# Kernel optimization log

Hardware: AMD Instinct MI355X
Metric: run time of the kernel (lower is better)

The kernel has to match this reference:

```python
import jax, jax.numpy as jnp
import numpy as np

N = 20000      # nodes
DEG = 16       # uniform in-degree (edges sorted by destination)
F_IN = 96      # raw node feature dim
T_EMB = 32     # node-type embedding dim -> conv1 input = 128
H = 128        # hidden_channels == out_channels
N_TYPES = 8


def _lstm_agg(x_seq, w_ih, w_hh, b_ih, b_hh):
    """LSTMAggregation: run LSTM over each node's neighbor sequence, return last hidden. x_seq: [N, T, F] -> [N, F]."""
    n = x_seq.shape[0]
    hdim = w_hh.shape[1]
    h0 = jnp.zeros((n, hdim), x_seq.dtype)
    bias = b_ih + b_hh

    def step(carry, x_t):
        h, c = carry
        gates = x_t @ w_ih.T + h @ w_hh.T + bias  # [N, 4H], torch gate order i,f,g,o
        i, f, g, o = jnp.split(gates, 4, axis=-1)
        i = jax.nn.sigmoid(i)
        f = jax.nn.sigmoid(f)
        g = jnp.tanh(g)
        o = jax.nn.sigmoid(o)
        c = f * c + i * g
        h = o * jnp.tanh(c)
        return (h, c), None

    (h, _), _ = jax.lax.scan(step, (h0, h0), jnp.swapaxes(x_seq, 0, 1))
    return h


def _sage_lstm(x, src, params):
    """SAGEConv with aggr='lstm': out = lin_l(LSTM_agg(x_j)) + lin_r(x)."""
    w_ih, w_hh, b_ih, b_hh, w_l, b_l, w_r = params
    # dst = repeat(arange(N), DEG) (sorted), so grouping neighbors per node is a reshape
    x_j = x[src].reshape(x.shape[0], DEG, x.shape[1])  # gather: [N, DEG, F]
    agg = _lstm_agg(x_j, w_ih, w_hh, b_ih, b_hh)
    return agg @ w_l.T + b_l + x @ w_r.T


def setup_inputs() -> dict:
    key = jax.random.key(0)
    ks = jax.random.split(key, 40)

    def rn(i, shape, s=0.05):
        return (jax.random.normal(ks[i], shape, jnp.float32) * s)

    inp = {
        "x": rn(0, (N, F_IN), 1.0),
        "node_type_ids": jax.random.randint(ks[1], (N,), 0, N_TYPES),
        "edge_src": jax.random.randint(ks[2], (N * DEG,), 0, N),
        "edge_dst": jnp.repeat(jnp.arange(N), DEG),
        "type_emb": rn(3, (N_TYPES, T_EMB)),
    }
    k = 4
    for l in (1, 2, 3):
        inp[f"w_ih{l}"] = rn(k, (4 * H, H)); k += 1
        inp[f"w_hh{l}"] = rn(k, (4 * H, H)); k += 1
        inp[f"b_ih{l}"] = rn(k, (4 * H,)); k += 1
        inp[f"b_hh{l}"] = rn(k, (4 * H,)); k += 1
        inp[f"w_l{l}"] = rn(k, (H, H)); k += 1
        inp[f"b_l{l}"] = rn(k, (H,)); k += 1
        inp[f"w_r{l}"] = rn(k, (H, H)); k += 1
    return inp


def reference(x, node_type_ids, edge_src, edge_dst, type_emb,
              w_ih1, w_hh1, b_ih1, b_hh1, w_l1, b_l1, w_r1,
              w_ih2, w_hh2, b_ih2, b_hh2, w_l2, b_l2, w_r2,
              w_ih3, w_hh3, b_ih3, b_hh3, w_l3, b_l3, w_r3):
    del edge_dst  # sortedness/uniform degree encoded in the reshape
    h = jnp.concatenate([x, type_emb[node_type_ids]], axis=1)  # [N, 128]
    h = jax.nn.relu(_sage_lstm(h, edge_src, (w_ih1, w_hh1, b_ih1, b_hh1, w_l1, b_l1, w_r1)))  # dropout = identity (eval)
    h = jax.nn.relu(_sage_lstm(h, edge_src, (w_ih2, w_hh2, b_ih2, b_hh2, w_l2, b_l2, w_r2)))
    h = _sage_lstm(h, edge_src, (w_ih3, w_hh3, b_ih3, b_hh3, w_l3, b_l3, w_r3))
    return h
```

## Files before the change

kernel.cpp:

```cpp
#include <hip/hip_runtime.h>

#define NN 20000
#define DEG 16
#define HDIM 128
#define GDIM 512

typedef __attribute__((ext_vector_type(8))) short bf16x8;
typedef __attribute__((ext_vector_type(4))) float f32x4;
typedef __attribute__((ext_vector_type(2))) unsigned u32x2;
typedef __attribute__((ext_vector_type(4))) unsigned u32x4;
typedef unsigned long long ull;

#define L2E  1.4426950408889634f
#define L2E2 2.8853900817779268f

__device__ __forceinline__ f32x4 mfma16(bf16x8 a, bf16x8 b, f32x4 c) {
    return __builtin_amdgcn_mfma_f32_16x16x32_bf16(a, b, c, 0, 0, 0);
}

__device__ __forceinline__ unsigned short f2bf(float f) {
    unsigned u = __builtin_bit_cast(unsigned, f);
    u += 0x7FFFu + ((u >> 16) & 1u);
    return (unsigned short)(u >> 16);
}

__device__ __forceinline__ unsigned cvtpk(float lo, float hi) {
    unsigned r;
    asm("v_cvt_pk_bf16_f32 %0, %1, %2" : "=v"(r) : "v"(lo), "v"(hi));
    return r;
}

__device__ __forceinline__ float bfhi(unsigned u) { return __builtin_bit_cast(float, u & 0xFFFF0000u); }
__device__ __forceinline__ float bflo(unsigned u) { return __builtin_bit_cast(float, u << 16); }

__device__ __forceinline__ void barrier_lgkm() {
    asm volatile("s_waitcnt lgkmcnt(0)\ns_barrier" ::: "memory");
}

__device__ __forceinline__ float sig_pre(float x) {
    return __builtin_amdgcn_rcpf(1.f + __builtin_amdgcn_exp2f(-x));
}
__device__ __forceinline__ float tanh_pre2(float x2) {
    return 1.f - 2.f * __builtin_amdgcn_rcpf(__builtin_amdgcn_exp2f(x2) + 1.f);
}

struct CvtArgs {
    const float *wih[3], *whh[3], *wl[3], *wr[3], *bih[3], *bhh[3];
    unsigned short *dih[3], *dhh[3], *dl[3], *dr[3];
    float *dbias[3];
};

__global__ __launch_bounds__(256) void cvt_kernel(CvtArgs a) {
    int l = blockIdx.x / 642, b = blockIdx.x % 642, t = threadIdx.x;
    if (b < 256) {
        int i = b * 256 + t;
        float s = ((i >> 14) == 2) ? L2E2 : L2E;
        a.dih[l][i] = f2bf(a.wih[l][i] * s);
    } else if (b < 512) {
        int i = (b - 256) * 256 + t;
        float s = ((i >> 14) == 2) ? L2E2 : L2E;
        a.dhh[l][i] = f2bf(a.whh[l][i] * s);
    } else if (b < 576) {
        int i = (b - 512) * 256 + t;
        a.dl[l][i] = f2bf(a.wl[l][i]);
    } else if (b < 640) {
        int i = (b - 576) * 256 + t;
        a.dr[l][i] = f2bf(a.wr[l][i]);
    } else {
        int i = (b - 640) * 256 + t;
        float s = ((i >> 7) == 2) ? L2E2 : L2E;
        a.dbias[l][i] = (a.bih[l][i] + a.bhh[l][i]) * s;
    }
}

__device__ __forceinline__ void phaseA2(const unsigned short (*htile)[136],
        const unsigned short* __restrict__ wih, const float* __restrict__ biasc,
        unsigned short* __restrict__ xihb, int mbase, int cl, int qh, int k8, int wv) {
    bf16x8 a0[4], a1[4];
#pragma unroll
    for (int kt = 0; kt < 4; ++kt) {
        a0[kt] = *(const bf16x8*)(&htile[cl][kt * 32 + k8]);
        a1[kt] = *(const bf16x8*)(&htile[16 + cl][kt * 32 + k8]);
    }
#pragma unroll
    for (int nt = 0; nt < 2; ++nt) {
        const int col = wv * 32 + nt * 16 + cl;
        f32x4 acc0[4], acc1[4];
#pragma unroll
        for (int g = 0; g < 4; ++g) {
            acc0[g] = (f32x4){0.f, 0.f, 0.f, 0.f};
            acc1[g] = (f32x4){0.f, 0.f, 0.f, 0.f};
        }
#pragma unroll
        for (int g = 0; g < 4; ++g)
#pragma unroll
            for (int kt = 0; kt < 4; ++kt) {
                bf16x8 b = *(const bf16x8*)(wih + (g * 128 + col) * HDIM + kt * 32 + k8);
                acc0[g] = mfma16(a0[kt], b, acc0[g]);
                acc1[g] = mfma16(a1[kt], b, acc1[g]);
            }
        float bias[4];
#pragma unroll
        for (int g = 0; g < 4; ++g) bias[g] = biasc[g * 128 + col];
#pragma unroll
        for (int r = 0; r < 4; ++r) {
            unsigned p0 = cvtpk(acc0[0][r] + bias[0], acc0[1][r] + bias[1]);
            unsigned p1 = cvtpk(acc0[2][r] + bias[2], acc0[3][r] + bias[3]);
            *(ull*)(xihb + (size_t)(mbase + qh * 4 + r) * GDIM + col * 4) =
                (ull)p0 | ((ull)p1 << 32);
            unsigned q0 = cvtpk(acc1[0][r] + bias[0], acc1[1][r] + bias[1]);
            unsigned q1 = cvtpk(acc1[2][r] + bias[2], acc1[3][r] + bias[3]);
            *(ull*)(xihb + (size_t)(mbase + 16 + qh * 4 + r) * GDIM + col * 4) =
                (ull)q0 | ((ull)q1 << 32);
        }
    }
}

__global__ __launch_bounds__(256) void gemmA0_kernel(
        const float* __restrict__ x, const int* __restrict__ types,
        const float* __restrict__ emb, const unsigned short* __restrict__ wih,
        const float* __restrict__ biasc, unsigned short* __restrict__ h0,
        unsigned short* __restrict__ xihb) {
    __shared__ unsigned short htile[32][136];
    const int tid = threadIdx.x;
    const int lane = tid & 63, wv = tid >> 6;
    const int cl = lane & 15, qh = lane >> 4, k8 = qh * 8;
    const int mbase = blockIdx.x * 32;

    const int row = tid >> 3, c0 = (tid & 7) * 16;
    f32x4 u[4];
    if (c0 < 96) {
#pragma unroll
        for (int j = 0; j < 4; ++j)
            u[j] = *(const f32x4*)(x + (size_t)(mbase + row) * 96 + c0 + 4 * j);
    } else {
        int ty = types[mbase + row];
#pragma unroll
        for (int j = 0; j < 4; ++j)
            u[j] = *(const f32x4*)(emb + ty * 32 + (c0 - 96) + 4 * j);
    }
    u32x4 pk, pk2;
    pk[0]  = cvtpk(u[0][0], u[0][1]); pk[1]  = cvtpk(u[0][2], u[0][3]);
    pk[2]  = cvtpk(u[1][0], u[1][1]); pk[3]  = cvtpk(u[1][2], u[1][3]);
    pk2[0] = cvtpk(u[2][0], u[2][1]); pk2[1] = cvtpk(u[2][2], u[2][3]);
    pk2[2] = cvtpk(u[3][0], u[3][1]); pk2[3] = cvtpk(u[3][2], u[3][3]);
    *(u32x4*)(&htile[row][c0]) = pk;
    *(u32x4*)(&htile[row][c0 + 8]) = pk2;
    *(u32x4*)(h0 + (size_t)(mbase + row) * HDIM + c0) = pk;
    *(u32x4*)(h0 + (size_t)(mbase + row) * HDIM + c0 + 8) = pk2;
    __syncthreads();

    phaseA2(htile, wih, biasc, xihb, mbase, cl, qh, k8, wv);
}

__global__ __launch_bounds__(512, 2) void lstm_kernel(
        const unsigned short* __restrict__ xihb, const unsigned short* __restrict__ whh,
        const int* __restrict__ esrc, unsigned short* __restrict__ agg) {
    __shared__ unsigned short hbuf[2][16][136];
    __shared__ unsigned srcs_t[256];

    const int tid = threadIdx.x;
    const int lane = tid & 63, wv = tid >> 6;
    const int cl = lane & 15, qh = lane >> 4, k8 = qh * 8;
    const int colb = wv * 16 + cl;
    const int base = blockIdx.x * 16;

    if (tid < 256)
        srcs_t[(tid & 15) * 16 + (tid >> 4)] = ((unsigned)esrc[base * DEG + tid]) << 10;

    const unsigned short* wp = whh + colb * HDIM + k8;
#define LDW(kt, g) (*(const bf16x8*)(wp + (g) * 128 * HDIM + (kt) * 32))
    bf16x8 w00 = LDW(0,0), w01 = LDW(0,1), w02 = LDW(0,2), w03 = LDW(0,3);
    bf16x8 w10 = LDW(1,0), w11 = LDW(1,1), w12 = LDW(1,2), w13 = LDW(1,3);
    bf16x8 w20 = LDW(2,0), w21 = LDW(2,1), w22 = LDW(2,2), w23 = LDW(2,3);
    bf16x8 w30 = LDW(3,0), w31 = LDW(3,1), w32 = LDW(3,2), w33 = LDW(3,3);
#undef LDW
    __syncthreads();

    const char* xp = (const char*)xihb + (size_t)colb * 8u;
    float c0 = 0.f, c1 = 0.f, c2 = 0.f, c3 = 0.f;
    unsigned pk0 = 0, pk1 = 0;
    ull xa0, xa1, xa2, xa3, xb0, xb1, xb2, xb3;

#define GATH(T, X0, X1, X2, X3) { \
    u32x4 sv = *(const u32x4*)&srcs_t[(T) * 16 + qh * 4]; \
    X0 = *(const ull*)(xp + sv[0]); \
    X1 = *(const ull*)(xp + sv[1]); \
    X2 = *(const ull*)(xp + sv[2]); \
    X3 = *(const ull*)(xp + sv[3]); }

    GATH(0, xa0, xa1, xa2, xa3)
    GATH(1, xb0, xb1, xb2, xb3)

#define STEP(T, X0, X1, X2, X3) { \
    f32x4 a0, a1, a2, a3; \
    { unsigned lo = (unsigned)X0, hi = (unsigned)(X0 >> 32); \
      a0[0] = bflo(lo); a1[0] = bfhi(lo); a2[0] = bflo(hi); a3[0] = bfhi(hi); } \
    { unsigned lo = (unsigned)X1, hi = (unsigned)(X1 >> 32); \
      a0[1] = bflo(lo); a1[1] = bfhi(lo); a2[1] = bflo(hi); a3[1] = bfhi(hi); } \
    { unsigned lo = (unsigned)X2, hi = (unsigned)(X2 >> 32); \
      a0[2] = bflo(lo); a1[2] = bfhi(lo); a2[2] = bflo(hi); a3[2] = bfhi(hi); } \
    { unsigned lo = (unsigned)X3, hi = (unsigned)(X3 >> 32); \
      a0[3] = bflo(lo); a1[3] = bfhi(lo); a2[3] = bflo(hi); a3[3] = bfhi(hi); } \
    if ((T) < 14) { GATH((T) + 2, X0, X1, X2, X3) } \
    if ((T) > 0) { \
        const unsigned short* hrow = &hbuf[((T) + 1) & 1][cl][k8]; \
        bf16x8 h0 = *(const bf16x8*)(hrow); \
        bf16x8 h1 = *(const bf16x8*)(hrow + 32); \
        bf16x8 h2 = *(const bf16x8*)(hrow + 64); \
        bf16x8 h3 = *(const bf16x8*)(hrow + 96); \
        a0 = mfma16(h0, w00, a0); a0 = mfma16(h1, w10, a0); \
        a0 = mfma16(h2, w20, a0); a0 = mfma16(h3, w30, a0); \
        a1 = mfma16(h0, w01, a1); a1 = mfma16(h1, w11, a1); \
        a1 = mfma16(h2, w21, a1); a1 = mfma16(h3, w31, a1); \
        a2 = mfma16(h0, w02, a2); a2 = mfma16(h1, w12, a2); \
        a2 = mfma16(h2, w22, a2); a2 = mfma16(h3, w32, a2); \
        a3 = mfma16(h0, w03, a3); a3 = mfma16(h1, w13, a3); \
        a3 = mfma16(h2, w23, a3); a3 = mfma16(h3, w33, a3); \
    } \
    float i0 = sig_pre(a0[0]), f0 = sig_pre(a1[0]), g0 = tanh_pre2(a2[0]), o0 = sig_pre(a3[0]); \
    c0 = f0 * c0 + i0 * g0; float hv0 = o0 * tanh_pre2(c0 * L2E2); \
    float i1 = sig_pre(a0[1]), f1 = sig_pre(a1[1]), g1 = tanh_pre2(a2[1]), o1 = sig_pre(a3[1]); \
    c1 = f1 * c1 + i1 * g1; float hv1 = o1 * tanh_pre2(c1 * L2E2); \
    float i2 = sig_pre(a0[2]), f2 = sig_pre(a1[2]), g2 = tanh_pre2(a2[2]), o2 = sig_pre(a3[2]); \
    c2 = f2 * c2 + i2 * g2; float hv2 = o2 * tanh_pre2(c2 * L2E2); \
    float i3 = sig_pre(a0[3]), f3 = sig_pre(a1[3]), g3 = tanh_pre2(a2[3]), o3 = sig_pre(a3[3]); \
    c3 = f3 * c3 + i3 * g3; float hv3 = o3 * tanh_pre2(c3 * L2E2); \
    pk0 = cvtpk(hv0, hv1); \
    pk1 = cvtpk(hv2, hv3); \
    if ((T) < 15) { \
        unsigned short* hp = &hbuf[(T) & 1][qh * 4][colb]; \
        hp[0]   = (unsigned short)pk0; \
        hp[136] = (unsigned short)(pk0 >> 16); \
        hp[272] = (unsigned short)pk1; \
        hp[408] = (unsigned short)(pk1 >> 16); \
        barrier_lgkm(); \
    } }

    STEP(0,  xa0, xa1, xa2, xa3)
    STEP(1,  xb0, xb1, xb2, xb3)
    STEP(2,  xa0, xa1, xa2, xa3)
    STEP(3,  xb0, xb1, xb2, xb3)
    STEP(4,  xa0, xa1, xa2, xa3)
    STEP(5,  xb0, xb1, xb2, xb3)
    STEP(6,  xa0, xa1, xa2, xa3)
    STEP(7,  xb0, xb1, xb2, xb3)
    STEP(8,  xa0, xa1, xa2, xa3)
    STEP(9,  xb0, xb1, xb2, xb3)
    STEP(10, xa0, xa1, xa2, xa3)
    STEP(11, xb0, xb1, xb2, xb3)
    STEP(12, xa0, xa1, xa2, xa3)
    STEP(13, xb0, xb1, xb2, xb3)
    STEP(14, xa0, xa1, xa2, xa3)
    STEP(15, xb0, xb1, xb2, xb3)
#undef STEP
#undef GATH

    unsigned short* ap = agg + (size_t)(base + qh * 4) * HDIM + colb;
    ap[0]   = (unsigned short)pk0;
    ap[128] = (unsigned short)(pk0 >> 16);
    ap[256] = (unsigned short)pk1;
    ap[384] = (unsigned short)(pk1 >> 16);
}

__global__ __launch_bounds__(256) void gemmCA_kernel(
        const unsigned short* __restrict__ agg, const unsigned short* __restrict__ hcur,
        const unsigned short* __restrict__ wl, const unsigned short* __restrict__ wr,
        const float* __restrict__ bl, const unsigned short* __restrict__ wih,
        const float* __restrict__ biasc, unsigned short* __restrict__ hnext,
        unsigned short* __restrict__ xihb) {
    __shared__ unsigned short htile[32][136];
    const int lane = threadIdx.x & 63, wv = threadIdx.x >> 6;
    const int cl = lane & 15, qh = lane >> 4, k8 = qh * 8;
    const int mbase = blockIdx.x * 32;

    bf16x8 bA0[4], bA1[4], bH0[4], bH1[4];
#pragma unroll
    for (int kt = 0; kt < 4; ++kt) {
        bA0[kt] = *(const bf16x8*)(agg  + (size_t)(mbase + cl) * HDIM + kt * 32 + k8);
        bA1[kt] = *(const bf16x8*)(agg  + (size_t)(mbase + 16 + cl) * HDIM + kt * 32 + k8);
        bH0[kt] = *(const bf16x8*)(hcur + (size_t)(mbase + cl) * HDIM + kt * 32 + k8);
        bH1[kt] = *(const bf16x8*)(hcur + (size_t)(mbase + 16 + cl) * HDIM + kt * 32 + k8);
    }
#pragma unroll
    for (int nt = 0; nt < 2; ++nt) {
        const int col = wv * 32 + nt * 16 + cl;
        f32x4 acc0 = {0.f, 0.f, 0.f, 0.f}, acc1 = {0.f, 0.f, 0.f, 0.f};
#pragma unroll
        for (int kt = 0; kt < 4; ++kt) {
            bf16x8 w = *(const bf16x8*)(wl + col * HDIM + kt * 32 + k8);
            acc0 = mfma16(bA0[kt], w, acc0);
            acc1 = mfma16(bA1[kt], w, acc1);
        }
#pragma unroll
        for (int kt = 0; kt < 4; ++kt) {
            bf16x8 w = *(const bf16x8*)(wr + col * HDIM + kt * 32 + k8);
            acc0 = mfma16(bH0[kt], w, acc0);
            acc1 = mfma16(bH1[kt], w, acc1);
        }
        float bias = bl[col];
#pragma unroll
        for (int r = 0; r < 4; ++r) {
            unsigned short v0 = f2bf(fmaxf(acc0[r] + bias, 0.f));
            unsigned short v1 = f2bf(fmaxf(acc1[r] + bias, 0.f));
            hnext[(size_t)(mbase + qh * 4 + r) * HDIM + col] = v0;
            hnext[(size_t)(mbase + 16 + qh * 4 + r) * HDIM + col] = v1;
            htile[qh * 4 + r][col] = v0;
            htile[16 + qh * 4 + r][col] = v1;
        }
    }
    __syncthreads();

    phaseA2(htile, wih, biasc, xihb, mbase, cl, qh, k8, wv);
}

__global__ __launch_bounds__(256) void gemmCF_kernel(
        const unsigned short* __restrict__ agg, const unsigned short* __restrict__ hcur,
        const unsigned short* __restrict__ wl, const unsigned short* __restrict__ wr,
        const float* __restrict__ bl, float* __restrict__ fout) {
    const int lane = threadIdx.x & 63, wv = threadIdx.x >> 6;
    const int cl = lane & 15, qh = lane >> 4, k8 = qh * 8;
    const int mbase = blockIdx.x * 32;

    bf16x8 bA0[4], bA1[4], bH0[4], bH1[4];
#pragma unroll
    for (int kt = 0; kt < 4; ++kt) {
        bA0[kt] = *(const bf16x8*)(agg  + (size_t)(mbase + cl) * HDIM + kt * 32 + k8);
        bA1[kt] = *(const bf16x8*)(agg  + (size_t)(mbase + 16 + cl) * HDIM + kt * 32 + k8);
        bH0[kt] = *(const bf16x8*)(hcur + (size_t)(mbase + cl) * HDIM + kt * 32 + k8);
        bH1[kt] = *(const bf16x8*)(hcur + (size_t)(mbase + 16 + cl) * HDIM + kt * 32 + k8);
    }
#pragma unroll
    for (int nt = 0; nt < 2; ++nt) {
        const int col = wv * 32 + nt * 16 + cl;
        f32x4 acc0 = {0.f, 0.f, 0.f, 0.f}, acc1 = {0.f, 0.f, 0.f, 0.f};
#pragma unroll
        for (int kt = 0; kt < 4; ++kt) {
            bf16x8 w = *(const bf16x8*)(wl + col * HDIM + kt * 32 + k8);
            acc0 = mfma16(bA0[kt], w, acc0);
            acc1 = mfma16(bA1[kt], w, acc1);
        }
#pragma unroll
        for (int kt = 0; kt < 4; ++kt) {
            bf16x8 w = *(const bf16x8*)(wr + col * HDIM + kt * 32 + k8);
            acc0 = mfma16(bH0[kt], w, acc0);
            acc1 = mfma16(bH1[kt], w, acc1);
        }
        float bias = bl[col];
#pragma unroll
        for (int r = 0; r < 4; ++r) {
            fout[(size_t)(mbase + qh * 4 + r) * HDIM + col] = acc0[r] + bias;
            fout[(size_t)(mbase + 16 + qh * 4 + r) * HDIM + col] = acc1[r] + bias;
        }
    }
}

extern "C" void kernel_launch(void* const* d_in, const int* in_sizes, int n_in,
                              void* d_out, int out_size, void* d_ws, size_t ws_size,
                              hipStream_t stream) {
    (void)in_sizes; (void)n_in; (void)out_size; (void)ws_size;

    const float* x     = (const float*)d_in[0];
    const int*   types = (const int*)d_in[1];
    const int*   esrc  = (const int*)d_in[2];
    const float* emb   = (const float*)d_in[4];

    char* ws = (char*)d_ws;
    unsigned short* hA   = (unsigned short*)ws; ws += (size_t)NN * HDIM * 2;
    unsigned short* hB   = (unsigned short*)ws; ws += (size_t)NN * HDIM * 2;
    unsigned short* agg  = (unsigned short*)ws; ws += (size_t)NN * HDIM * 2;
    unsigned short* xihb = (unsigned short*)ws; ws += (size_t)NN * GDIM * 2;
    unsigned short* wbf  = (unsigned short*)ws; ws += (size_t)3 * 163840 * 2;
    float*          bc   = (float*)ws;

    unsigned short *wihb[3], *whhb[3], *wlb[3], *wrb[3];
    float* bcl[3];
    CvtArgs ca;
    for (int l = 0; l < 3; ++l) {
        unsigned short* lb = wbf + (size_t)l * 163840;
        wihb[l] = lb;
        whhb[l] = lb + 65536;
        wlb[l]  = lb + 131072;
        wrb[l]  = lb + 147456;
        bcl[l]  = bc + l * 512;
        ca.wih[l] = (const float*)d_in[5 + 7 * l + 0];
        ca.whh[l] = (const float*)d_in[5 + 7 * l + 1];
        ca.bih[l] = (const float*)d_in[5 + 7 * l + 2];
        ca.bhh[l] = (const float*)d_in[5 + 7 * l + 3];
        ca.wl[l]  = (const float*)d_in[5 + 7 * l + 4];
        ca.wr[l]  = (const float*)d_in[5 + 7 * l + 6];
        ca.dih[l] = wihb[l]; ca.dhh[l] = whhb[l]; ca.dl[l] = wlb[l]; ca.dr[l] = wrb[l];
        ca.dbias[l] = bcl[l];
    }
    cvt_kernel<<<1926, 256, 0, stream>>>(ca);

    gemmA0_kernel<<<NN / 32, 256, 0, stream>>>(x, types, emb, wihb[0], bcl[0], hA, xihb);

    unsigned short* hc = hA;
    unsigned short* hn = hB;
    for (int l = 0; l < 3; ++l) {
        const float* bl = (const float*)d_in[5 + 7 * l + 5];
        lstm_kernel<<<NN / 16, 512, 0, stream>>>(xihb, whhb[l], esrc, agg);
        if (l < 2) {
            gemmCA_kernel<<<NN / 32, 256, 0, stream>>>(
                agg, hc, wlb[l], wrb[l], bl, wihb[l + 1], bcl[l + 1], hn, xihb);
            unsigned short* t = hc; hc = hn; hn = t;
        } else {
            gemmCF_kernel<<<NN / 32, 256, 0, stream>>>(
                agg, hc, wlb[l], wrb[l], bl, (float*)d_out);
        }
    }
}
```

Baseline: 305.7 us.

## Halve LSTM block to 256 threads, two column tiles per wave

The LSTM recurrence kernel now runs 4 waves per block instead of 8, with each wave covering two 16-column hidden tiles (A and B). That doubles the gather loads, MFMAs and nonlinearities per wave. W_hh fragments are no longer held in registers; they are reloaded from global memory each step through the WA/WB macros. The aim is to cut per-step barrier cost, since fewer waves sync each step, and to raise ILP per wave, at the cost of repeated weight loads from cache and higher register pressure.

```diff
diff --git a/kernel.cpp b/kernel.cpp
--- a/kernel.cpp
+++ b/kernel.cpp
@@ -153,7 +153,7 @@
     phaseA2(htile, wih, biasc, xihb, mbase, cl, qh, k8, wv);
 }
 
-__global__ __launch_bounds__(512, 2) void lstm_kernel(
+__global__ __launch_bounds__(256, 4) void lstm_kernel(
         const unsigned short* __restrict__ xihb, const unsigned short* __restrict__ whh,
         const int* __restrict__ esrc, unsigned short* __restrict__ agg) {
     __shared__ unsigned short hbuf[2][16][136];
@@ -162,105 +162,136 @@
     const int tid = threadIdx.x;
     const int lane = tid & 63, wv = tid >> 6;
     const int cl = lane & 15, qh = lane >> 4, k8 = qh * 8;
-    const int colb = wv * 16 + cl;
+    const int colA = wv * 32 + cl;
     const int base = blockIdx.x * 16;
 
-    if (tid < 256)
-        srcs_t[(tid & 15) * 16 + (tid >> 4)] = ((unsigned)esrc[base * DEG + tid]) << 10;
-
-    const unsigned short* wp = whh + colb * HDIM + k8;
-#define LDW(kt, g) (*(const bf16x8*)(wp + (g) * 128 * HDIM + (kt) * 32))
-    bf16x8 w00 = LDW(0,0), w01 = LDW(0,1), w02 = LDW(0,2), w03 = LDW(0,3);
-    bf16x8 w10 = LDW(1,0), w11 = LDW(1,1), w12 = LDW(1,2), w13 = LDW(1,3);
-    bf16x8 w20 = LDW(2,0), w21 = LDW(2,1), w22 = LDW(2,2), w23 = LDW(2,3);
-    bf16x8 w30 = LDW(3,0), w31 = LDW(3,1), w32 = LDW(3,2), w33 = LDW(3,3);
-#undef LDW
+    srcs_t[(tid & 15) * 16 + (tid >> 4)] = ((unsigned)esrc[base * DEG + tid]) << 10;
     __syncthreads();
 
-    const char* xp = (const char*)xihb + (size_t)colb * 8u;
+    const unsigned short* wpA = whh + colA * HDIM + k8;
+    const unsigned short* wpB = wpA + 16 * HDIM;
+#define WA(g, kt) (*(const bf16x8*)(wpA + (g) * 128 * HDIM + (kt) * 32))
+#define WB(g, kt) (*(const bf16x8*)(wpB + (g) * 128 * HDIM + (kt) * 32))
+
+    const char* xpA = (const char*)xihb + (size_t)colA * 8u;
+    const char* xpB = xpA + 128;
     float c0 = 0.f, c1 = 0.f, c2 = 0.f, c3 = 0.f;
-    unsigned pk0 = 0, pk1 = 0;
-    ull xa0, xa1, xa2, xa3, xb0, xb1, xb2, xb3;
-
-#define GATH(T, X0, X1, X2, X3) { \
+    float c4 = 0.f, c5 = 0.f, c6 = 0.f, c7 = 0.f;
+    unsigned pkA0 = 0, pkA1 = 0, pkB0 = 0, pkB1 = 0;
+    ull ya0, ya1, ya2, ya3, ya4, ya5, ya6, ya7;
+    ull yb0, yb1, yb2, yb3, yb4, yb5, yb6, yb7;
+
+#define GATH(T, X0, X1, X2, X3, X4, X5, X6, X7) { \
     u32x4 sv = *(const u32x4*)&srcs_t[(T) * 16 + qh * 4]; \
-    X0 = *(const ull*)(xp + sv[0]); \
-    X1 = *(const ull*)(xp + sv[1]); \
-    X2 = *(const ull*)(xp + sv[2]); \
-    X3 = *(const ull*)(xp + sv[3]); }
-
-    GATH(0, xa0, xa1, xa2, xa3)
-    GATH(1, xb0, xb1, xb2, xb3)
-
-#define STEP(T, X0, X1, X2, X3) { \
-    f32x4 a0, a1, a2, a3; \
+    X0 = *(const ull*)(xpA + sv[0]); \
+    X1 = *(const ull*)(xpA + sv[1]); \
+    X2 = *(const ull*)(xpA + sv[2]); \
+    X3 = *(const ull*)(xpA + sv[3]); \
+    X4 = *(const ull*)(xpB + sv[0]); \
+    X5 = *(const ull*)(xpB + sv[1]); \
+    X6 = *(const ull*)(xpB + sv[2]); \
+    X7 = *(const ull*)(xpB + sv[3]); }
+
+    GATH(0, ya0, ya1, ya2, ya3, ya4, ya5, ya6, ya7)
+    GATH(1, yb0, yb1, yb2, yb3, yb4, yb5, yb6, yb7)
+
+#define UNP(X0, X1, X2, X3, A0, A1, A2, A3) \
     { unsigned lo = (unsigned)X0, hi = (unsigned)(X0 >> 32); \
-      a0[0] = bflo(lo); a1[0] = bfhi(lo); a2[0] = bflo(hi); a3[0] = bfhi(hi); } \
+      A0[0] = bflo(lo); A1[0] = bfhi(lo); A2[0] = bflo(hi); A3[0] = bfhi(hi); } \
     { unsigned lo = (unsigned)X1, hi = (unsigned)(X1 >> 32); \
-      a0[1] = bflo(lo); a1[1] = bfhi(lo); a2[1] = bflo(hi); a3[1] = bfhi(hi); } \
+      A0[1] = bflo(lo); A1[1] = bfhi(lo); A2[1] = bflo(hi); A3[1] = bfhi(hi); } \
     { unsigned lo = (unsigned)X2, hi = (unsigned)(X2 >> 32); \
-      a0[2] = bflo(lo); a1[2] = bfhi(lo); a2[2] = bflo(hi); a3[2] = bfhi(hi); } \
+      A0[2] = bflo(lo); A1[2] = bfhi(lo); A2[2] = bflo(hi); A3[2] = bfhi(hi); } \
     { unsigned lo = (unsigned)X3, hi = (unsigned)(X3 >> 32); \
-      a0[3] = bflo(lo); a1[3] = bfhi(lo); a2[3] = bflo(hi); a3[3] = bfhi(hi); } \
-    if ((T) < 14) { GATH((T) + 2, X0, X1, X2, X3) } \
+      A0[3] = bflo(lo); A1[3] = bfhi(lo); A2[3] = bflo(hi); A3[3] = bfhi(hi); }
+
+#define NONLIN(A0, A1, A2, A3, C0, C1, C2, C3, PK0, PK1) { \
+    float i0 = sig_pre(A0[0]), f0 = sig_pre(A1[0]), g0 = tanh_pre2(A2[0]), o0 = sig_pre(A3[0]); \
+    C0 = f0 * C0 + i0 * g0; float hv0 = o0 * tanh_pre2(C0 * L2E2); \
+    float i1 = sig_pre(A0[1]), f1 = sig_pre(A1[1]), g1 = tanh_pre2(A2[1]), o1 = sig_pre(A3[1]); \
+    C1 = f1 * C1 + i1 * g1; float hv1 = o1 * tanh_pre2(C1 * L2E2); \
+    float i2 = sig_pre(A0[2]), f2 = sig_pre(A1[2]), g2 = tanh_pre2(A2[2]), o2 = sig_pre(A3[2]); \
+    C2 = f2 * C2 + i2 * g2; float hv2 = o2 * tanh_pre2(C2 * L2E2); \
+    float i3 = sig_pre(A0[3]), f3 = sig_pre(A1[3]), g3 = tanh_pre2(A2[3]), o3 = sig_pre(A3[3]); \
+    C3 = f3 * C3 + i3 * g3; float hv3 = o3 * tanh_pre2(C3 * L2E2); \
+    PK0 = cvtpk(hv0, hv1); \
+    PK1 = cvtpk(hv2, hv3); }
+
+#define STEP(T, X0, X1, X2, X3, X4, X5, X6, X7) { \
+    f32x4 aA0, aA1, aA2, aA3, aB0, aB1, aB2, aB3; \
+    UNP(X0, X1, X2, X3, aA0, aA1, aA2, aA3) \
+    UNP(X4, X5, X6, X7, aB0, aB1, aB2, aB3) \
+    if ((T) < 14) { GATH((T) + 2, X0, X1, X2, X3, X4, X5, X6, X7) } \
     if ((T) > 0) { \
         const unsigned short* hrow = &hbuf[((T) + 1) & 1][cl][k8]; \
         bf16x8 h0 = *(const bf16x8*)(hrow); \
         bf16x8 h1 = *(const bf16x8*)(hrow + 32); \
         bf16x8 h2 = *(const bf16x8*)(hrow + 64); \
         bf16x8 h3 = *(const bf16x8*)(hrow + 96); \
-        a0 = mfma16(h0, w00, a0); a0 = mfma16(h1, w10, a0); \
-        a0 = mfma16(h2, w20, a0); a0 = mfma16(h3, w30, a0); \
-        a1 = mfma16(h0, w01, a1); a1 = mfma16(h1, w11, a1); \
-        a1 = mfma16(h2, w21, a1); a1 = mfma16(h3, w31, a1); \
-        a2 = mfma16(h0, w02, a2); a2 = mfma16(h1, w12, a2); \
-        a2 = mfma16(h2, w22, a2); a2 = mfma16(h3, w32, a2); \
-        a3 = mfma16(h0, w03, a3); a3 = mfma16(h1, w13, a3); \
-        a3 = mfma16(h2, w23, a3); a3 = mfma16(h3, w33, a3); \
+        aA0 = mfma16(h0, WA(0,0), aA0); aA0 = mfma16(h1, WA(0,1), aA0); \
+        aA0 = mfma16(h2, WA(0,2), aA0); aA0 = mfma16(h3, WA(0,3), aA0); \
+        aA1 = mfma16(h0, WA(1,0), aA1); aA1 = mfma16(h1, WA(1,1), aA1); \
+        aA1 = mfma16(h2, WA(1,2), aA1); aA1 = mfma16(h3, WA(1,3), aA1); \
+        aA2 = mfma16(h0, WA(2,0), aA2); aA2 = mfma16(h1, WA(2,1), aA2); \
+        aA2 = mfma16(h2, WA(2,2), aA2); aA2 = mfma16(h3, WA(2,3), aA2); \
+        aA3 = mfma16(h0, WA(3,0), aA3); aA3 = mfma16(h1, WA(3,1), aA3); \
+        aA3 = mfma16(h2, WA(3,2), aA3); aA3 = mfma16(h3, WA(3,3), aA3); \
+        aB0 = mfma16(h0, WB(0,0), aB0); aB0 = mfma16(h1, WB(0,1), aB0); \
+        aB0 = mfma16(h2, WB(0,2), aB0); aB0 = mfma16(h3, WB(0,3), aB0); \
+        aB1 = mfma16(h0, WB(1,0), aB1); aB1 = mfma16(h1, WB(1,1), aB1); \
+        aB1 = mfma16(h2, WB(1,2), aB1); aB1 = mfma16(h3, WB(1,3), aB1); \
+        aB2 = mfma16(h0, WB(2,0), aB2); aB2 = mfma16(h1, WB(2,1), aB2); \
+        aB2 = mfma16(h2, WB(2,2), aB2); aB2 = mfma16(h3, WB(2,3), aB2); \
+        aB3 = mfma16(h0, WB(3,0), aB3); aB3 = mfma16(h1, WB(3,1), aB3); \
+        aB3 = mfma16(h2, WB(3,2), aB3); aB3 = mfma16(h3, WB(3,3), aB3); \
     } \
-    float i0 = sig_pre(a0[0]), f0 = sig_pre(a1[0]), g0 = tanh_pre2(a2[0]), o0 = sig_pre(a3[0]); \
-    c0 = f0 * c0 + i0 * g0; float hv0 = o0 * tanh_pre2(c0 * L2E2); \
-    float i1 = sig_pre(a0[1]), f1 = sig_pre(a1[1]), g1 = tanh_pre2(a2[1]), o1 = sig_pre(a3[1]); \
-    c1 = f1 * c1 + i1 * g1; float hv1 = o1 * tanh_pre2(c1 * L2E2); \
-    float i2 = sig_pre(a0[2]), f2 = sig_pre(a1[2]), g2 = tanh_pre2(a2[2]), o2 = sig_pre(a3[2]); \
-    c2 = f2 * c2 + i2 * g2; float hv2 = o2 * tanh_pre2(c2 * L2E2); \
-    float i3 = sig_pre(a0[3]), f3 = sig_pre(a1[3]), g3 = tanh_pre2(a2[3]), o3 = sig_pre(a3[3]); \
-    c3 = f3 * c3 + i3 * g3; float hv3 = o3 * tanh_pre2(c3 * L2E2); \
-    pk0 = cvtpk(hv0, hv1); \
-    pk1 = cvtpk(hv2, hv3); \
+    NONLIN(aA0, aA1, aA2, aA3, c0, c1, c2, c3, pkA0, pkA1) \
+    NONLIN(aB0, aB1, aB2, aB3, c4, c5, c6, c7, pkB0, pkB1) \
     if ((T) < 15) { \
-        unsigned short* hp = &hbuf[(T) & 1][qh * 4][colb]; \
-        hp[0]   = (unsigned short)pk0; \
-        hp[136] = (unsigned short)(pk0 >> 16); \
-        hp[272] = (unsigned short)pk1; \
-        hp[408] = (unsigned short)(pk1 >> 16); \
+        unsigned short* hp = &hbuf[(T) & 1][qh * 4][colA]; \
+        hp[0]        = (unsigned short)pkA0; \
+        hp[136]      = (unsigned short)(pkA0 >> 16); \
+        hp[272]      = (unsigned short)pkA1; \
+        hp[408]      = (unsigned short)(pkA1 >> 16); \
+        hp[16]       = (unsigned short)pkB0; \
+        hp[136 + 16] = (unsigned short)(pkB0 >> 16); \
+        hp[272 + 16] = (unsigned short)pkB1; \
+        hp[408 + 16] = (unsigned short)(pkB1 >> 16); \
         barrier_lgkm(); \
     } }
 
-    STEP(0,  xa0, xa1, xa2, xa3)
-    STEP(1,  xb0, xb1, xb2, xb3)
-    STEP(2,  xa0, xa1, xa2, xa3)
-    STEP(3,  xb0, xb1, xb2, xb3)
-    STEP(4,  xa0, xa1, xa2, xa3)
-    STEP(5,  xb0, xb1, xb2, xb3)
-    STEP(6,  xa0, xa1, xa2, xa3)
-    STEP(7,  xb0, xb1, xb2, xb3)
-    STEP(8,  xa0, xa1, xa2, xa3)
-    STEP(9,  xb0, xb1, xb2, xb3)
-    STEP(10, xa0, xa1, xa2, xa3)
-    STEP(11, xb0, xb1, xb2, xb3)
-    STEP(12, xa0, xa1, xa2, xa3)
-    STEP(13, xb0, xb1, xb2, xb3)
-    STEP(14, xa0, xa1, xa2, xa3)
-    STEP(15, xb0, xb1, xb2, xb3)
+    STEP(0,  ya0, ya1, ya2, ya3, ya4, ya5, ya6, ya7)
+    STEP(1,  yb0, yb1, yb2, yb3, yb4, yb5, yb6, yb7)
+    STEP(2,  ya0, ya1, ya2, ya3, ya4, ya5, ya6, ya7)
+    STEP(3,  yb0, yb1, yb2, yb3, yb4, yb5, yb6, yb7)
+    STEP(4,  ya0, ya1, ya2, ya3, ya4, ya5, ya6, ya7)
+    STEP(5,  yb0, yb1, yb2, yb3, yb4, yb5, yb6, yb7)
+    STEP(6,  ya0, ya1, ya2, ya3, ya4, ya5, ya6, ya7)
+    STEP(7,  yb0, yb1, yb2, yb3, yb4, yb5, yb6, yb7)
+    STEP(8,  ya0, ya1, ya2, ya3, ya4, ya5, ya6, ya7)
+    STEP(9,  yb0, yb1, yb2, yb3, yb4, yb5, yb6, yb7)
+    STEP(10, ya0, ya1, ya2, ya3, ya4, ya5, ya6, ya7)
+    STEP(11, yb0, yb1, yb2, yb3, yb4, yb5, yb6, yb7)
+    STEP(12, ya0, ya1, ya2, ya3, ya4, ya5, ya6, ya7)
+    STEP(13, yb0, yb1, yb2, yb3, yb4, yb5, yb6, yb7)
+    STEP(14, ya0, ya1, ya2, ya3, ya4, ya5, ya6, ya7)
+    STEP(15, yb0, yb1, yb2, yb3, yb4, yb5, yb6, yb7)
 #undef STEP
+#undef NONLIN
+#undef UNP
 #undef GATH
-
-    unsigned short* ap = agg + (size_t)(base + qh * 4) * HDIM + colb;
-    ap[0]   = (unsigned short)pk0;
-    ap[128] = (unsigned short)(pk0 >> 16);
-    ap[256] = (unsigned short)pk1;
-    ap[384] = (unsigned short)(pk1 >> 16);
+#undef WA
+#undef WB
+
+    unsigned short* ap = agg + (size_t)(base + qh * 4) * HDIM + colA;
+    ap[0]        = (unsigned short)pkA0;
+    ap[128]      = (unsigned short)(pkA0 >> 16);
+    ap[256]      = (unsigned short)pkA1;
+    ap[384]      = (unsigned short)(pkA1 >> 16);
+    ap[16]       = (unsigned short)pkB0;
+    ap[128 + 16] = (unsigned short)(pkB0 >> 16);
+    ap[256 + 16] = (unsigned short)pkB1;
+    ap[384 + 16] = (unsigned short)(pkB1 >> 16);
 }
 
 __global__ __launch_bounds__(256) void gemmCA_kernel(
@@ -400,7 +431,7 @@
     unsigned short* hn = hB;
     for (int l = 0; l < 3; ++l) {
         const float* bl = (const float*)d_in[5 + 7 * l + 5];
-        lstm_kernel<<<NN / 16, 512, 0, stream>>>(xihb, whhb[l], esrc, agg);
+        lstm_kernel<<<NN / 16, 256, 0, stream>>>(xihb, whhb[l], esrc, agg);
         if (l < 2) {
             gemmCA_kernel<<<NN / 32, 256, 0, stream>>>(
                 agg, hc, wlb[l], wrb[l], bl, wihb[l + 1], bcl[l + 1], hn, xihb);
```

Result: slower. 989.5 us (+223.6%).
